# Kernel tuning notes

Measured on AMD Instinct MI355X. Metric: run time of the kernel, lower is better.

Reference implementation:

```python
import jax, jax.numpy as jnp
import numpy as np

FORMULA_OH_SIZES = [20, 20, 20, 20, 20]
SPECT_BIN_N = 512


def layer_norm(x, g, b, eps=1e-5):
    m = jnp.mean(x, axis=-1, keepdims=True)
    v = jnp.var(x, axis=-1, keepdims=True)
    return (x - m) * jax.lax.rsqrt(v + eps) * g + b


def gru_cell(x, h, W_ih, W_hh, b_ih, b_hh):
    # torch.nn.GRUCell math
    gi = x @ W_ih.T + b_ih
    gh = h @ W_hh.T + b_hh
    i_r, i_z, i_n = jnp.split(gi, 3, axis=-1)
    h_r, h_z, h_n = jnp.split(gh, 3, axis=-1)
    r = jax.nn.sigmoid(i_r + h_r)
    z = jax.nn.sigmoid(i_z + h_z)
    n = jnp.tanh(i_n + r * h_n)
    return (1.0 - z) * n + z * h


def structured_one_hot(x, sizes, accum=True):
    # x: [N, len(sizes)] integer element counts -> concatenated (accumulated) one-hots
    outs = []
    for i, s in enumerate(sizes):
        v = jnp.clip(x[:, i].astype(jnp.int32), 0, s - 1)
        if accum:
            oh = (jnp.arange(s)[None, :] <= v[:, None]).astype(jnp.float32)  # thermometer
        else:
            oh = jax.nn.one_hot(v, s, dtype=jnp.float32)
        outs.append(oh)
    return jnp.concatenate(outs, axis=-1)


def setup_inputs():
    key = jax.random.key(0)
    ks = jax.random.split(key, 16)
    B, A, GF, HW, S, M = 16, 32, 128, 4, 4096, 8
    G = GF * HW                       # 512 = g_feat_in * highway_steps_n
    FE = sum(FORMULA_OH_SIZES)        # 100
    D = 512                           # internal_d
    vert_feat_in = jax.random.normal(ks[0], (B, A, GF, HW), jnp.float32)
    vert_mask_in = jnp.ones((B, A), jnp.float32)
    elem_id = jax.random.randint(ks[1], (B, A), 0, 5)
    vert_element_oh = jax.nn.one_hot(elem_id, 5, dtype=jnp.float32)
    adj_oh = jnp.zeros((B, A, A, 4), jnp.float32)  # unused by forward
    atom_subsets = jax.random.bernoulli(ks[2], 0.5, (B, S, A)).astype(jnp.float32)
    masses = jax.random.uniform(ks[3], (B, S, M), jnp.float32, 0.0, SPECT_BIN_N - 1.0)
    intens = jax.random.uniform(ks[4], (B, S, M), jnp.float32)
    atom_subsets_peaks = jnp.stack([masses, intens], axis=-1)

    def lin(k, o, i):
        return (jax.random.normal(k, (o, i), jnp.float32) / np.sqrt(i)).astype(jnp.float32)

    return dict(
        vert_feat_in=vert_feat_in, vert_mask_in=vert_mask_in,
        vert_element_oh=vert_element_oh, adj_oh=adj_oh,
        atom_subsets=atom_subsets, atom_subsets_peaks=atom_subsets_peaks,
        ln_sub_g=jnp.ones((G,), jnp.float32), ln_sub_b=jnp.zeros((G,), jnp.float32),
        W_ih=lin(ks[5], 3 * G, FE), W_hh=lin(ks[6], 3 * G, G),
        b_ih=jnp.zeros((3 * G,), jnp.float32), b_hh=jnp.zeros((3 * G,), jnp.float32),
        W1=lin(ks[7], D, G), b1=jnp.zeros((D,), jnp.float32),
        W2a=lin(ks[8], D, D), b2a=jnp.zeros((D,), jnp.float32),
        W2b=lin(ks[9], D, D), b2b=jnp.zeros((D,), jnp.float32),
        ln_pre_g=jnp.ones((D,), jnp.float32), ln_pre_b=jnp.zeros((D,), jnp.float32),
        Ws=lin(ks[10], 1, D), bs=jnp.zeros((1,), jnp.float32),
    )


def reference(vert_feat_in, vert_mask_in, vert_element_oh, adj_oh, atom_subsets,
              atom_subsets_peaks, ln_sub_g, ln_sub_b, W_ih, W_hh, b_ih, b_hh,
              W1, b1, W2a, b2a, W2b, b2b, ln_pre_g, ln_pre_b, Ws, bs):
    B, A, GF, HW = vert_feat_in.shape
    S = atom_subsets.shape[1]
    vf = vert_feat_in.reshape(B, A, GF * HW)                       # [B,A,G]
    masked_vf = vf * vert_mask_in[:, :, None]
    subs_m = atom_subsets * vert_mask_in[:, None, :]               # [B,S,A]
    swvs = jnp.einsum('bag,bsa->bsg', masked_vf, subs_m)           # [B,S,G]
    # per-subset element counts -> structured one-hot formula encoding
    counts = jnp.einsum('bae,bsa->bse', vert_element_oh, atom_subsets).astype(jnp.int32)
    pf_flat = structured_one_hot(counts.reshape(B * S, -1), FORMULA_OH_SIZES, accum=True)
    subset_size = jnp.sum(subs_m, axis=2) + 1e-4                   # [B,S]
    mean = swvs / subset_size[:, :, None]
    normed = layer_norm(mean, ln_sub_g, ln_sub_b)                  # [B,S,G]
    h = gru_cell(pf_flat, normed.reshape(B * S, -1), W_ih, W_hh, b_ih, b_hh)
    h = h.reshape(normed.shape)
    x = jax.nn.relu(h @ W1.T + b1)
    x = jax.nn.relu(x @ W2a.T + b2a)
    x = jax.nn.relu(x @ W2b.T + b2b)   # (extra F.relu in original is idempotent)
    x = layer_norm(x, ln_pre_g, ln_pre_b)
    scores = (x @ Ws.T + bs)[..., 0]                               # [B,S]
    probs = jax.nn.softmax(scores, axis=-1)
    # mass histogram: scatter intensity*prob into rounded-mass bins
    masses = atom_subsets_peaks[..., 0]                            # [B,S,M]
    intens = atom_subsets_peaks[..., 1]
    bins = jnp.clip(jnp.round(masses).astype(jnp.int32), 0, SPECT_BIN_N - 1)
    contrib = intens * probs[:, :, None]                           # [B,S,M]
    spect = jnp.zeros((B, SPECT_BIN_N), x.dtype).at[
        jnp.arange(B)[:, None], bins.reshape(B, -1)].add(contrib.reshape(B, -1))
    return (spect, probs)
```

## Files before the change

### kernel.cpp

```cpp
#include <hip/hip_runtime.h>
#include <math.h>

#define B_ 16
#define A_ 32
#define G_ 512
#define S_ 4096
#define M_ 8
#define BS_ 65536
#define KC_ 640
#define NG_ 1536

typedef _Float16 half8 __attribute__((ext_vector_type(8)));
typedef _Float16 half4v __attribute__((ext_vector_type(4)));
typedef _Float16 half2v __attribute__((ext_vector_type(2)));
typedef float floatx4 __attribute__((ext_vector_type(4)));

typedef const __attribute__((address_space(1))) void* gas_t;
typedef __attribute__((address_space(3))) void* las_t;

__device__ __forceinline__ float wave_sum_f(float v){
#pragma unroll
  for (int o = 32; o > 0; o >>= 1) v += __shfl_xor(v, o);
  return v;
}
__device__ __forceinline__ float wave_max_f(float v){
#pragma unroll
  for (int o = 32; o > 0; o >>= 1) v = fmaxf(v, __shfl_xor(v, o));
  return v;
}
__device__ __forceinline__ float sigmoidf_(float x){ return 1.f/(1.f+__expf(-x)); }
__device__ __forceinline__ float tanhf_(float x){ return 1.f - 2.f/(__expf(2.f*x)+1.f); }

__global__ __launch_bounds__(256) void k_cvt3(const float* __restrict__ s0,
                                              const float* __restrict__ s1,
                                              const float* __restrict__ s2,
                                              _Float16* __restrict__ d){
  const float* s = (blockIdx.y == 0) ? s0 : (blockIdx.y == 1) ? s1 : s2;
  int i = (blockIdx.x*256 + threadIdx.x)*4;
  if (i >= G_*G_) return;
  float4 v = *(const float4*)(s+i);
  half4v o; o[0]=(_Float16)v.x; o[1]=(_Float16)v.y; o[2]=(_Float16)v.z; o[3]=(_Float16)v.w;
  *(half4v*)(d + (size_t)blockIdx.y*G_*G_ + i) = o;
}

__global__ __launch_bounds__(64) void k_buildw(const float* __restrict__ Whh,
                                               const float* __restrict__ Wih,
                                               _Float16* __restrict__ Wcat){
  int j = blockIdx.x;
  for (int p = threadIdx.x; p < KC_; p += 64){
    float v = 0.f;
    if (p < 512) v = Whh[(size_t)j*512 + p];
    else if (p < 612) v = Wih[(size_t)j*100 + (p - 512)];
    Wcat[(size_t)j*KC_ + p] = (_Float16)v;
  }
}

__global__ __launch_bounds__(256) void k_prep_mfma(
    const float* __restrict__ vf, const float* __restrict__ mask,
    const float* __restrict__ eoh, const float* __restrict__ subs,
    const float* __restrict__ ln_g, const float* __restrict__ ln_b,
    _Float16* __restrict__ Abuf){
  __shared__ _Float16 s_mvfT[G_*A_];
  __shared__ _Float16 s_sm[128*A_];
  __shared__ float s_m[A_];
  __shared__ float s_e[A_*5];
  __shared__ float s_ssum[128];
  __shared__ float s_red1[2][4][16];
  __shared__ float s_red2[2][4][16];
  int tid = threadIdx.x;
  int bx = blockIdx.x, b = blockIdx.y;
  int lane = tid & 63, w = tid >> 6;
  int q = lane >> 4, l15 = lane & 15;
  size_t row0 = (size_t)b*S_ + (size_t)bx*128;
  if (tid < A_)   s_m[tid] = mask[b*A_ + tid];
  if (tid < A_*5) s_e[tid] = eoh[b*A_*5 + tid];
  __syncthreads();
  {
    int p = tid & 15, gseg = tid >> 4;
    float mk0 = s_m[2*p], mk1 = s_m[2*p+1];
    const float* v0 = vf + ((size_t)b*A_ + 2*p)*G_ + gseg*32;
    const float* v1 = v0 + G_;
#pragma unroll
    for (int i = 0; i < 32; i += 4){
      float4 a = *(const float4*)(v0 + i);
      float4 c = *(const float4*)(v1 + i);
      float av[4] = {a.x, a.y, a.z, a.w};
      float cv[4] = {c.x, c.y, c.z, c.w};
#pragma unroll
      for (int j = 0; j < 4; ++j){
        half2v h; h[0] = (_Float16)(av[j]*mk0); h[1] = (_Float16)(cv[j]*mk1);
        *(half2v*)(s_mvfT + (gseg*32 + i + j)*A_ + 2*p) = h;
      }
    }
  }
  {
    int s = tid >> 1, hh = tid & 1;
    const float* sp = subs + (row0 + s)*A_ + hh*16;
    _Float16* dst = s_sm + s*A_ + hh*16;
#pragma unroll
    for (int i = 0; i < 16; i += 4){
      float4 v = *(const float4*)(sp + i);
      half4v h; h[0]=(_Float16)v.x; h[1]=(_Float16)v.y; h[2]=(_Float16)v.z; h[3]=(_Float16)v.w;
      *(half4v*)(dst + i) = h;
    }
  }
  __syncthreads();
  if (tid < 128){
    int s = tid;
    float ssum = 0.f, c0=0.f, c1=0.f, c2=0.f, c3=0.f, c4=0.f;
#pragma unroll
    for (int a = 0; a < A_; ++a){
      float v = (float)s_sm[s*A_ + a];
      ssum += v * s_m[a];
      c0 += v * s_e[a*5+0]; c1 += v * s_e[a*5+1]; c2 += v * s_e[a*5+2];
      c3 += v * s_e[a*5+3]; c4 += v * s_e[a*5+4];
    }
    int cc[5];
    cc[0] = min(max((int)(c0+0.5f),0),19); cc[1] = min(max((int)(c1+0.5f),0),19);
    cc[2] = min(max((int)(c2+0.5f),0),19); cc[3] = min(max((int)(c3+0.5f),0),19);
    cc[4] = min(max((int)(c4+0.5f),0),19);
    s_ssum[s] = ssum;
    _Float16* dst = Abuf + (row0 + s)*KC_ + 512;
#pragma unroll
    for (int t = 0; t < 16; ++t){
      half8 hv;
#pragma unroll
      for (int u = 0; u < 8; ++u){
        int k = t*8 + u;
        float v = 0.f;
        if (k < 100){ int f = k/20, l = k - f*20; v = (l <= cc[f]) ? 1.f : 0.f; }
        hv[u] = (_Float16)v;
      }
      *(half8*)(dst + t*8) = hv;
    }
  }
  half8 bf[8]; float lng[8], lnb[8];
#pragma unroll
  for (int t = 0; t < 8; ++t){
    int g = w*128 + t*16 + l15;
    bf[t] = *(const half8*)(s_mvfT + g*A_ + q*8);
    lng[t] = ln_g[g]; lnb[t] = ln_b[g];
  }
  __syncthreads();
  for (int gi = 0; gi < 8; ++gi){
    half8 af = *(const half8*)(s_sm + (gi*16 + l15)*A_ + q*8);
    floatx4 c[8];
#pragma unroll
    for (int t = 0; t < 8; ++t){
      floatx4 z = {0.f, 0.f, 0.f, 0.f};
      c[t] = __builtin_amdgcn_mfma_f32_16x16x32_f16(af, bf[t], z, 0, 0, 0);
    }
    float p1[4] = {0.f,0.f,0.f,0.f}, p2[4] = {0.f,0.f,0.f,0.f};
#pragma unroll
    for (int t = 0; t < 8; ++t)
#pragma unroll
      for (int r = 0; r < 4; ++r){ float v = c[t][r]; p1[r] += v; p2[r] += v*v; }
#pragma unroll
    for (int off = 1; off < 16; off <<= 1)
#pragma unroll
      for (int r = 0; r < 4; ++r){
        p1[r] += __shfl_xor(p1[r], off);
        p2[r] += __shfl_xor(p2[r], off);
      }
    int gb = gi & 1;
    if (l15 == 0){
#pragma unroll
      for (int r = 0; r < 4; ++r){ s_red1[gb][w][q*4+r] = p1[r]; s_red2[gb][w][q*4+r] = p2[r]; }
    }
    __syncthreads();
#pragma unroll
    for (int r = 0; r < 4; ++r){
      int sl = gi*16 + q*4 + r;
      int rr = q*4 + r;
      float t1 = s_red1[gb][0][rr] + s_red1[gb][1][rr] + s_red1[gb][2][rr] + s_red1[gb][3][rr];
      float t2 = s_red2[gb][0][rr] + s_red2[gb][1][rr] + s_red2[gb][2][rr] + s_red2[gb][3][rr];
      float inv = 1.f/(s_ssum[sl] + 1e-4f);
      float mu = t1*inv*(1.f/512.f);
      float var = t2*inv*inv*(1.f/512.f) - mu*mu;
      float rs = rsqrtf(var + 1e-5f);
      _Float16* orow = Abuf + (row0 + sl)*KC_;
#pragma unroll
      for (int t = 0; t < 8; ++t){
        float o = (c[t][r]*inv - mu)*rs*lng[t] + lnb[t];
        orow[w*128 + t*16 + l15] = (_Float16)o;
      }
    }
  }
}

__global__ __launch_bounds__(512) void k_gru_fused(
    const _Float16* __restrict__ Abuf, const _Float16* __restrict__ Wcat,
    const float* __restrict__ bih, const float* __restrict__ bhh,
    _Float16* __restrict__ H){
  __shared__ _Float16 smA[128*32];
  __shared__ _Float16 smB[192*32];
  int tid = threadIdx.x;
  int lane = tid & 63, wvid = tid >> 6;
  int wm = wvid & 1, wn = wvid >> 1;
  int q = lane >> 4, l15 = lane & 15;
  int mt = blockIdx.x*64 + (blockIdx.y >> 3);
  int dt = blockIdx.y & 7;
  int m0 = mt*128, n0 = dt*64;
  floatx4 acc[3][4] = {};
  floatx4 accNI[4] = {};
  int offA[4], offB[3];
#pragma unroll
  for (int i = 0; i < 4; ++i){
    int r = wm*64 + i*16 + l15;
    offA[i] = (r*4 + (q ^ ((r>>2)&3)))*8;
  }
#pragma unroll
  for (int g = 0; g < 3; ++g){
    int rb = g*64 + wn*16 + l15;
    offB[g] = (rb*4 + (q ^ ((rb>>2)&3)))*8;
  }
  const _Float16* gA;
  {
    int u = wvid*64 + lane;
    int r = u >> 2, c = (u & 3) ^ ((r >> 2) & 3);
    gA = Abuf + (size_t)(m0 + r)*KC_ + c*8;
  }
  const _Float16* gB0;
  {
    int u = wvid*64 + lane;
    int rb = u >> 2, c = (u & 3) ^ ((rb >> 2) & 3);
    int grow = (rb >> 6)*512 + n0 + (rb & 63);
    gB0 = Wcat + (size_t)grow*KC_ + c*8;
  }
  const _Float16* gB1 = nullptr;
  if (wvid < 4){
    int u = (8 + wvid)*64 + lane;
    int rb = u >> 2, c = (u & 3) ^ ((rb >> 2) & 3);
    int grow = (rb >> 6)*512 + n0 + (rb & 63);
    gB1 = Wcat + (size_t)grow*KC_ + c*8;
  }
  for (int kc = 0; kc < 512; kc += 32){
    __builtin_amdgcn_global_load_lds((gas_t)(gA + kc), (las_t)(smA + wvid*512), 16, 0, 0);
    __builtin_amdgcn_global_load_lds((gas_t)(gB0 + kc), (las_t)(smB + wvid*512), 16, 0, 0);
    if (wvid < 4)
      __builtin_amdgcn_global_load_lds((gas_t)(gB1 + kc), (las_t)(smB + (8+wvid)*512), 16, 0, 0);
    __syncthreads();
    half8 af[4], bfv[3];
#pragma unroll
    for (int i = 0; i < 4; ++i) af[i] = *(const half8*)(smA + offA[i]);
#pragma unroll
    for (int g = 0; g < 3; ++g) bfv[g] = *(const half8*)(smB + offB[g]);
#pragma unroll
    for (int g = 0; g < 3; ++g)
#pragma unroll
      for (int i = 0; i < 4; ++i)
        acc[g][i] = __builtin_amdgcn_mfma_f32_16x16x32_f16(af[i], bfv[g], acc[g][i], 0, 0, 0);
    __syncthreads();
  }
  for (int kc = 512; kc < KC_; kc += 32){
    __builtin_amdgcn_global_load_lds((gas_t)(gA + kc), (las_t)(smA + wvid*512), 16, 0, 0);
    __builtin_amdgcn_global_load_lds((gas_t)(gB0 + kc), (las_t)(smB + wvid*512), 16, 0, 0);
    if (wvid < 4)
      __builtin_amdgcn_global_load_lds((gas_t)(gB1 + kc), (las_t)(smB + (8+wvid)*512), 16, 0, 0);
    __syncthreads();
    half8 af[4], bfv[3];
#pragma unroll
    for (int i = 0; i < 4; ++i) af[i] = *(const half8*)(smA + offA[i]);
#pragma unroll
    for (int g = 0; g < 3; ++g) bfv[g] = *(const half8*)(smB + offB[g]);
#pragma unroll
    for (int i = 0; i < 4; ++i){
      acc[0][i] = __builtin_amdgcn_mfma_f32_16x16x32_f16(af[i], bfv[0], acc[0][i], 0, 0, 0);
      acc[1][i] = __builtin_amdgcn_mfma_f32_16x16x32_f16(af[i], bfv[1], acc[1][i], 0, 0, 0);
      accNI[i]  = __builtin_amdgcn_mfma_f32_16x16x32_f16(af[i], bfv[2], accNI[i], 0, 0, 0);
    }
    __syncthreads();
  }
  int d = n0 + wn*16 + l15;
  float br  = bih[d] + bhh[d];
  float bz  = bih[512+d] + bhh[512+d];
  float bnh = bhh[1024+d];
  float bni = bih[1024+d];
#pragma unroll
  for (int i = 0; i < 4; ++i){
#pragma unroll
    for (int r = 0; r < 4; ++r){
      int m = m0 + wm*64 + i*16 + q*4 + r;
      float gr  = acc[0][i][r] + br;
      float gz  = acc[1][i][r] + bz;
      float hn  = acc[2][i][r] + bnh;
      float in_ = accNI[i][r] + bni;
      float rrv = sigmoidf_(gr);
      float zz  = sigmoidf_(gz);
      float nn  = tanhf_(in_ + rrv*hn);
      float hp  = (float)Abuf[(size_t)m*KC_ + d];
      H[(size_t)m*G_ + d] = (_Float16)((1.f-zz)*nn + zz*hp);
    }
  }
}

__global__ __launch_bounds__(256) void k_gemm(
    const _Float16* __restrict__ A, const _Float16* __restrict__ W,
    const float* __restrict__ bias, _Float16* __restrict__ Out){
  __shared__ _Float16 smA[128*32];
  __shared__ _Float16 smB[128*32];
  int tid = threadIdx.x;
  int lane = tid & 63, wvid = tid >> 6;
  int wm = wvid & 1, wn = wvid >> 1;
  int q = lane >> 4, l15 = lane & 15;
  int mt = blockIdx.x*64 + (blockIdx.y >> 2);
  int nt = blockIdx.y & 3;
  int m0 = mt*128, n0 = nt*128;
  floatx4 acc[4][4] = {};
  int offA[4], offB[4];
#pragma unroll
  for (int i = 0; i < 4; ++i){
    int r = wm*64 + i*16 + l15;
    offA[i] = (r*4 + (q ^ ((r>>2)&3)))*8;
    int rb = wn*64 + i*16 + l15;
    offB[i] = (rb*4 + (q ^ ((rb>>2)&3)))*8;
  }
  int uA[2];
  const _Float16 *gA[2], *gB[2];
#pragma unroll
  for (int t = 0; t < 2; ++t){
    int seg = wvid*2 + t;
    int u = seg*64 + lane;
    int r = u >> 2, c = (u & 3) ^ ((r >> 2) & 3);
    uA[t] = seg;
    gA[t] = A + (size_t)(m0 + r)*G_ + c*8;
    gB[t] = W + (size_t)(n0 + r)*G_ + c*8;
  }
  for (int kc = 0; kc < G_; kc += 32){
#pragma unroll
    for (int t = 0; t < 2; ++t){
      __builtin_amdgcn_global_load_lds((gas_t)(gA[t] + kc), (las_t)(smA + uA[t]*512), 16, 0, 0);
      __builtin_amdgcn_global_load_lds((gas_t)(gB[t] + kc), (las_t)(smB + uA[t]*512), 16, 0, 0);
    }
    __syncthreads();
    half8 af[4], bfv[4];
#pragma unroll
    for (int i = 0; i < 4; ++i) af[i] = *(const half8*)(smA + offA[i]);
#pragma unroll
    for (int j = 0; j < 4; ++j) bfv[j] = *(const half8*)(smB + offB[j]);
#pragma unroll
    for (int i = 0; i < 4; ++i)
#pragma unroll
      for (int j = 0; j < 4; ++j)
        acc[i][j] = __builtin_amdgcn_mfma_f32_16x16x32_f16(af[i], bfv[j], acc[i][j], 0, 0, 0);
    __syncthreads();
  }
#pragma unroll
  for (int j = 0; j < 4; ++j){
    int n = n0 + wn*64 + j*16 + l15;
    float bv = bias[n];
#pragma unroll
    for (int i = 0; i < 4; ++i){
#pragma unroll
      for (int r = 0; r < 4; ++r){
        int m = m0 + wm*64 + i*16 + q*4 + r;
        Out[(size_t)m*G_ + n] = (_Float16)fmaxf(acc[i][j][r] + bv, 0.f);
      }
    }
  }
}

__global__ __launch_bounds__(256) void k_ff3_fin(
    const _Float16* __restrict__ A, const _Float16* __restrict__ W,
    const float* __restrict__ bias, const float* __restrict__ ln_pre_g,
    const float* __restrict__ Ws, float* __restrict__ Pbuf){
  __shared__ _Float16 smA[128*32];
  __shared__ _Float16 smB[128*32];
  __shared__ float sP[2][64][2][3];
  int tid = threadIdx.x;
  int lane = tid & 63, wvid = tid >> 6;
  int wm = wvid & 1, wn = wvid >> 1;
  int q = lane >> 4, l15 = lane & 15;
  int mt = blockIdx.x*64 + (blockIdx.y >> 2);
  int nt = blockIdx.y & 3;
  int m0 = mt*128, n0 = nt*128;
  floatx4 acc[4][4] = {};
  int offA[4], offB[4];
#pragma unroll
  for (int i = 0; i < 4; ++i){
    int r = wm*64 + i*16 + l15;
    offA[i] = (r*4 + (q ^ ((r>>2)&3)))*8;
    int rb = wn*64 + i*16 + l15;
    offB[i] = (rb*4 + (q ^ ((rb>>2)&3)))*8;
  }
  int uA[2];
  const _Float16 *gA[2], *gB[2];
#pragma unroll
  for (int t = 0; t < 2; ++t){
    int seg = wvid*2 + t;
    int u = seg*64 + lane;
    int r = u >> 2, c = (u & 3) ^ ((r >> 2) & 3);
    uA[t] = seg;
    gA[t] = A + (size_t)(m0 + r)*G_ + c*8;
    gB[t] = W + (size_t)(n0 + r)*G_ + c*8;
  }
  for (int kc = 0; kc < G_; kc += 32){
#pragma unroll
    for (int t = 0; t < 2; ++t){
      __builtin_amdgcn_global_load_lds((gas_t)(gA[t] + kc), (las_t)(smA + uA[t]*512), 16, 0, 0);
      __builtin_amdgcn_global_load_lds((gas_t)(gB[t] + kc), (las_t)(smB + uA[t]*512), 16, 0, 0);
    }
    __syncthreads();
    half8 af[4], bfv[4];
#pragma unroll
    for (int i = 0; i < 4; ++i) af[i] = *(const half8*)(smA + offA[i]);
#pragma unroll
    for (int j = 0; j < 4; ++j) bfv[j] = *(const half8*)(smB + offB[j]);
#pragma unroll
    for (int i = 0; i < 4; ++i)
#pragma unroll
      for (int j = 0; j < 4; ++j)
        acc[i][j] = __builtin_amdgcn_mfma_f32_16x16x32_f16(af[i], bfv[j], acc[i][j], 0, 0, 0);
    __syncthreads();
  }
  float gws[4], bv4[4];
#pragma unroll
  for (int j = 0; j < 4; ++j){
    int n = n0 + wn*64 + j*16 + l15;
    gws[j] = ln_pre_g[n]*Ws[n];
    bv4[j] = bias[n];
  }
#pragma unroll
  for (int i = 0; i < 4; ++i){
#pragma unroll
    for (int r = 0; r < 4; ++r){
      float p1 = 0.f, p2 = 0.f, p3 = 0.f;
#pragma unroll
      for (int j = 0; j < 4; ++j){
        float x = fmaxf(acc[i][j][r] + bv4[j], 0.f);
        p1 += x; p2 += x*x; p3 += gws[j]*x;
      }
#pragma unroll
      for (int off = 1; off < 16; off <<= 1){
        p1 += __shfl_xor(p1, off);
        p2 += __shfl_xor(p2, off);
        p3 += __shfl_xor(p3, off);
      }
      if (l15 == 0){
        int rl = i*16 + q*4 + r;
        sP[wm][rl][wn][0] = p1; sP[wm][rl][wn][1] = p2; sP[wm][rl][wn][2] = p3;
      }
    }
  }
  __syncthreads();
  if (tid < 128){
    int wmi = tid >> 6, rl = tid & 63;
    int m = m0 + wmi*64 + rl;
    float* dst = Pbuf + ((size_t)m*4 + nt)*3;
    dst[0] = sP[wmi][rl][0][0] + sP[wmi][rl][1][0];
    dst[1] = sP[wmi][rl][0][1] + sP[wmi][rl][1][1];
    dst[2] = sP[wmi][rl][0][2] + sP[wmi][rl][1][2];
  }
}

__global__ __launch_bounds__(256) void k_score_fin(
    const float* __restrict__ Pbuf, const float* __restrict__ g,
    const float* __restrict__ bta, const float* __restrict__ Ws,
    const float* __restrict__ bs, float* __restrict__ scores){
  __shared__ float red[8];
  int tid = threadIdx.x, lane = tid & 63, wv = tid >> 6;
  int i0 = tid*2;
  float c1p = g[i0]*Ws[i0] + g[i0+1]*Ws[i0+1];
  float c2p = bta[i0]*Ws[i0] + bta[i0+1]*Ws[i0+1];
  c1p = wave_sum_f(c1p); c2p = wave_sum_f(c2p);
  if (lane == 0){ red[wv] = c1p; red[4+wv] = c2p; }
  __syncthreads();
  float c1 = red[0]+red[1]+red[2]+red[3];
  float c2 = red[4]+red[5]+red[6]+red[7] + bs[0];
  size_t row = (size_t)blockIdx.x*256 + tid;
  const float* p = Pbuf + row*12;
  float4 a  = *(const float4*)p;
  float4 b4 = *(const float4*)(p+4);
  float4 c4 = *(const float4*)(p+8);
  float P1 = a.x + a.w + b4.z + c4.y;
  float P2 = a.y + b4.x + b4.w + c4.z;
  float P3 = a.z + b4.y + c4.x + c4.w;
  float mu = P1*(1.f/512.f);
  float var = P2*(1.f/512.f) - mu*mu;
  float rs = rsqrtf(var + 1e-5f);
  scores[row] = rs*(P3 - mu*c1) + c2;
}

__global__ __launch_bounds__(256) void k_softmax(
    const float* __restrict__ scores, float* __restrict__ probs){
  __shared__ float red[4];
  int b = blockIdx.x, tid = threadIdx.x, lane = tid & 63, wv = tid >> 6;
  const float* sp = scores + (size_t)b*S_;
  float mx = -1e30f;
  for (int i = tid; i < S_; i += 256) mx = fmaxf(mx, sp[i]);
  mx = wave_max_f(mx);
  if (lane == 0) red[wv] = mx;
  __syncthreads();
  mx = fmaxf(fmaxf(red[0], red[1]), fmaxf(red[2], red[3]));
  __syncthreads();
  float sum = 0.f;
  for (int i = tid; i < S_; i += 256) sum += __expf(sp[i]-mx);
  sum = wave_sum_f(sum);
  if (lane == 0) red[wv] = sum;
  __syncthreads();
  sum = red[0]+red[1]+red[2]+red[3];
  float inv = 1.f/sum;
  for (int i = tid; i < S_; i += 256)
    probs[(size_t)b*S_ + i] = __expf(sp[i]-mx)*inv;
}

__global__ __launch_bounds__(256) void k_spect(
    const float* __restrict__ peaks, const float* __restrict__ probs,
    float* __restrict__ spect){
  __shared__ float bins[512];
  int b = blockIdx.x, tid = threadIdx.x;
  bins[tid] = 0.f; bins[tid+256] = 0.f;
  __syncthreads();
  for (int i = tid; i < S_*M_; i += 256){
    int s = i >> 3, m = i & 7;
    const float* pk = peaks + (((size_t)b*S_ + s)*M_ + m)*2;
    float mass = pk[0], inten = pk[1];
    float p = probs[(size_t)b*S_ + s];
    int bin = (int)rintf(mass);
    bin = min(max(bin, 0), 511);
    atomicAdd(&bins[bin], inten*p);
  }
  __syncthreads();
  spect[(size_t)b*512 + tid]       = bins[tid];
  spect[(size_t)b*512 + tid + 256] = bins[tid+256];
}

extern "C" void kernel_launch(void* const* d_in, const int* in_sizes, int n_in,
                              void* d_out, int out_size, void* d_ws, size_t ws_size,
                              hipStream_t stream) {
  const float* vf       = (const float*)d_in[0];
  const float* mask     = (const float*)d_in[1];
  const float* eoh      = (const float*)d_in[2];
  const float* subs     = (const float*)d_in[4];
  const float* peaks    = (const float*)d_in[5];
  const float* ln_sub_g = (const float*)d_in[6];
  const float* ln_sub_b = (const float*)d_in[7];
  const float* W_ih     = (const float*)d_in[8];
  const float* W_hh     = (const float*)d_in[9];
  const float* b_ih     = (const float*)d_in[10];
  const float* b_hh     = (const float*)d_in[11];
  const float* W1       = (const float*)d_in[12];
  const float* b1       = (const float*)d_in[13];
  const float* W2a      = (const float*)d_in[14];
  const float* b2a      = (const float*)d_in[15];
  const float* W2b      = (const float*)d_in[16];
  const float* b2b      = (const float*)d_in[17];
  const float* ln_pre_g = (const float*)d_in[18];
  const float* ln_pre_b = (const float*)d_in[19];
  const float* Ws       = (const float*)d_in[20];
  const float* bs       = (const float*)d_in[21];
  float* out = (float*)d_out;
  float* probs_out = out + (size_t)B_*512;

  char* w = (char*)d_ws;
  float* scores = (float*)w;     w += (size_t)BS_*4;
  float* Pbuf   = (float*)w;     w += (size_t)BS_*12*4;
  _Float16* Wcat = (_Float16*)w; w += (size_t)NG_*KC_*2;
  _Float16* W1h  = (_Float16*)w; w += (size_t)G_*G_*2;
  _Float16* W2ah = (_Float16*)w; w += (size_t)G_*G_*2;
  _Float16* W2bh = (_Float16*)w; w += (size_t)G_*G_*2;
  _Float16* Abuf = (_Float16*)w; w += (size_t)BS_*KC_*2;
  _Float16* bufh0 = (_Float16*)w;
  _Float16* bufh1 = Abuf;

  k_cvt3<<<dim3((G_*G_/4+255)/256, 3), 256, 0, stream>>>(W1, W2a, W2b, W1h);
  k_buildw<<<NG_, 64, 0, stream>>>(W_hh, W_ih, Wcat);
  k_prep_mfma<<<dim3(S_/128, B_), 256, 0, stream>>>(vf, mask, eoh, subs,
                                                    ln_sub_g, ln_sub_b, Abuf);
  k_gru_fused<<<dim3(8, 512), 512, 0, stream>>>(Abuf, Wcat, b_ih, b_hh, bufh0);
  k_gemm<<<dim3(8, 256), 256, 0, stream>>>(bufh0, W1h,  b1,  bufh1);
  k_gemm<<<dim3(8, 256), 256, 0, stream>>>(bufh1, W2ah, b2a, bufh0);
  k_ff3_fin<<<dim3(8, 256), 256, 0, stream>>>(bufh0, W2bh, b2b,
                                              ln_pre_g, Ws, Pbuf);
  k_score_fin<<<BS_/256, 256, 0, stream>>>(Pbuf, ln_pre_g, ln_pre_b, Ws, bs, scores);
  k_softmax<<<B_, 256, 0, stream>>>(scores, probs_out);
  k_spect<<<B_, 256, 0, stream>>>(peaks, probs_out, out);
}
```

Baseline: 526.5 us.

## Use 8 waves per GEMM block and fuse score, softmax and spectrum kernels

The three FF GEMM kernels now run 512 threads (8 waves) per 128x128 tile, so each wave computes a 64x32 sub-tile and issues one LDS load per operand instead of two. This halves the accumulators per wave, which should lower register pressure and raise occupancy and latency hiding. Separately, the score finalisation, softmax and spectrum scatter are merged into one kernel per batch that keeps scores and probabilities in shared memory, removing two launches and a global scores buffer. The tradeoff is that score computation now runs in only 16 blocks instead of 256, so less of the GPU is busy for that stage.

```diff
diff --git a/kernel.cpp b/kernel.cpp
--- a/kernel.cpp
+++ b/kernel.cpp
@@ -294,7 +294,7 @@
   }
 }
 
-__global__ __launch_bounds__(256) void k_gemm(
+__global__ __launch_bounds__(512) void k_gemm(
     const _Float16* __restrict__ A, const _Float16* __restrict__ W,
     const float* __restrict__ bias, _Float16* __restrict__ Out){
   __shared__ _Float16 smA[128*32];
@@ -306,48 +306,44 @@
   int mt = blockIdx.x*64 + (blockIdx.y >> 2);
   int nt = blockIdx.y & 3;
   int m0 = mt*128, n0 = nt*128;
-  floatx4 acc[4][4] = {};
-  int offA[4], offB[4];
+  floatx4 acc[4][2] = {};
+  int offA[4], offB[2];
 #pragma unroll
   for (int i = 0; i < 4; ++i){
     int r = wm*64 + i*16 + l15;
     offA[i] = (r*4 + (q ^ ((r>>2)&3)))*8;
-    int rb = wn*64 + i*16 + l15;
-    offB[i] = (rb*4 + (q ^ ((rb>>2)&3)))*8;
-  }
-  int uA[2];
-  const _Float16 *gA[2], *gB[2];
-#pragma unroll
-  for (int t = 0; t < 2; ++t){
-    int seg = wvid*2 + t;
-    int u = seg*64 + lane;
+  }
+#pragma unroll
+  for (int j = 0; j < 2; ++j){
+    int rb = wn*32 + j*16 + l15;
+    offB[j] = (rb*4 + (q ^ ((rb>>2)&3)))*8;
+  }
+  const _Float16 *gA, *gB;
+  {
+    int u = wvid*64 + lane;
     int r = u >> 2, c = (u & 3) ^ ((r >> 2) & 3);
-    uA[t] = seg;
-    gA[t] = A + (size_t)(m0 + r)*G_ + c*8;
-    gB[t] = W + (size_t)(n0 + r)*G_ + c*8;
+    gA = A + (size_t)(m0 + r)*G_ + c*8;
+    gB = W + (size_t)(n0 + r)*G_ + c*8;
   }
   for (int kc = 0; kc < G_; kc += 32){
-#pragma unroll
-    for (int t = 0; t < 2; ++t){
-      __builtin_amdgcn_global_load_lds((gas_t)(gA[t] + kc), (las_t)(smA + uA[t]*512), 16, 0, 0);
-      __builtin_amdgcn_global_load_lds((gas_t)(gB[t] + kc), (las_t)(smB + uA[t]*512), 16, 0, 0);
-    }
-    __syncthreads();
-    half8 af[4], bfv[4];
+    __builtin_amdgcn_global_load_lds((gas_t)(gA + kc), (las_t)(smA + wvid*512), 16, 0, 0);
+    __builtin_amdgcn_global_load_lds((gas_t)(gB + kc), (las_t)(smB + wvid*512), 16, 0, 0);
+    __syncthreads();
+    half8 af[4], bfv[2];
 #pragma unroll
     for (int i = 0; i < 4; ++i) af[i] = *(const half8*)(smA + offA[i]);
 #pragma unroll
-    for (int j = 0; j < 4; ++j) bfv[j] = *(const half8*)(smB + offB[j]);
+    for (int j = 0; j < 2; ++j) bfv[j] = *(const half8*)(smB + offB[j]);
 #pragma unroll
     for (int i = 0; i < 4; ++i)
 #pragma unroll
-      for (int j = 0; j < 4; ++j)
+      for (int j = 0; j < 2; ++j)
         acc[i][j] = __builtin_amdgcn_mfma_f32_16x16x32_f16(af[i], bfv[j], acc[i][j], 0, 0, 0);
     __syncthreads();
   }
 #pragma unroll
-  for (int j = 0; j < 4; ++j){
-    int n = n0 + wn*64 + j*16 + l15;
+  for (int j = 0; j < 2; ++j){
+    int n = n0 + wn*32 + j*16 + l15;
     float bv = bias[n];
 #pragma unroll
     for (int i = 0; i < 4; ++i){
@@ -360,13 +356,13 @@
   }
 }
 
-__global__ __launch_bounds__(256) void k_ff3_fin(
+__global__ __launch_bounds__(512) void k_ff3_fin(
     const _Float16* __restrict__ A, const _Float16* __restrict__ W,
     const float* __restrict__ bias, const float* __restrict__ ln_pre_g,
     const float* __restrict__ Ws, float* __restrict__ Pbuf){
   __shared__ _Float16 smA[128*32];
   __shared__ _Float16 smB[128*32];
-  __shared__ float sP[2][64][2][3];
+  __shared__ float sP[2][64][4][3];
   int tid = threadIdx.x;
   int lane = tid & 63, wvid = tid >> 6;
   int wm = wvid & 1, wn = wvid >> 1;
@@ -374,51 +370,47 @@
   int mt = blockIdx.x*64 + (blockIdx.y >> 2);
   int nt = blockIdx.y & 3;
   int m0 = mt*128, n0 = nt*128;
-  floatx4 acc[4][4] = {};
-  int offA[4], offB[4];
+  floatx4 acc[4][2] = {};
+  int offA[4], offB[2];
 #pragma unroll
   for (int i = 0; i < 4; ++i){
     int r = wm*64 + i*16 + l15;
     offA[i] = (r*4 + (q ^ ((r>>2)&3)))*8;
-    int rb = wn*64 + i*16 + l15;
-    offB[i] = (rb*4 + (q ^ ((rb>>2)&3)))*8;
-  }
-  int uA[2];
-  const _Float16 *gA[2], *gB[2];
-#pragma unroll
-  for (int t = 0; t < 2; ++t){
-    int seg = wvid*2 + t;
-    int u = seg*64 + lane;
+  }
+#pragma unroll
+  for (int j = 0; j < 2; ++j){
+    int rb = wn*32 + j*16 + l15;
+    offB[j] = (rb*4 + (q ^ ((rb>>2)&3)))*8;
+  }
+  const _Float16 *gA, *gB;
+  {
+    int u = wvid*64 + lane;
     int r = u >> 2, c = (u & 3) ^ ((r >> 2) & 3);
-    uA[t] = seg;
-    gA[t] = A + (size_t)(m0 + r)*G_ + c*8;
-    gB[t] = W + (size_t)(n0 + r)*G_ + c*8;
+    gA = A + (size_t)(m0 + r)*G_ + c*8;
+    gB = W + (size_t)(n0 + r)*G_ + c*8;
   }
   for (int kc = 0; kc < G_; kc += 32){
-#pragma unroll
-    for (int t = 0; t < 2; ++t){
-      __builtin_amdgcn_global_load_lds((gas_t)(gA[t] + kc), (las_t)(smA + uA[t]*512), 16, 0, 0);
-      __builtin_amdgcn_global_load_lds((gas_t)(gB[t] + kc), (las_t)(smB + uA[t]*512), 16, 0, 0);
-    }
-    __syncthreads();
-    half8 af[4], bfv[4];
+    __builtin_amdgcn_global_load_lds((gas_t)(gA + kc), (las_t)(smA + wvid*512), 16, 0, 0);
+    __builtin_amdgcn_global_load_lds((gas_t)(gB + kc), (las_t)(smB + wvid*512), 16, 0, 0);
+    __syncthreads();
+    half8 af[4], bfv[2];
 #pragma unroll
     for (int i = 0; i < 4; ++i) af[i] = *(const half8*)(smA + offA[i]);
 #pragma unroll
-    for (int j = 0; j < 4; ++j) bfv[j] = *(const half8*)(smB + offB[j]);
+    for (int j = 0; j < 2; ++j) bfv[j] = *(const half8*)(smB + offB[j]);
 #pragma unroll
     for (int i = 0; i < 4; ++i)
 #pragma unroll
-      for (int j = 0; j < 4; ++j)
+      for (int j = 0; j < 2; ++j)
         acc[i][j] = __builtin_amdgcn_mfma_f32_16x16x32_f16(af[i], bfv[j], acc[i][j], 0, 0, 0);
     __syncthreads();
   }
-  float gws[4], bv4[4];
-#pragma unroll
-  for (int j = 0; j < 4; ++j){
-    int n = n0 + wn*64 + j*16 + l15;
+  float gws[2], bv2[2];
+#pragma unroll
+  for (int j = 0; j < 2; ++j){
+    int n = n0 + wn*32 + j*16 + l15;
     gws[j] = ln_pre_g[n]*Ws[n];
-    bv4[j] = bias[n];
+    bv2[j] = bias[n];
   }
 #pragma unroll
   for (int i = 0; i < 4; ++i){
@@ -426,8 +418,8 @@
     for (int r = 0; r < 4; ++r){
       float p1 = 0.f, p2 = 0.f, p3 = 0.f;
 #pragma unroll
-      for (int j = 0; j < 4; ++j){
-        float x = fmaxf(acc[i][j][r] + bv4[j], 0.f);
+      for (int j = 0; j < 2; ++j){
+        float x = fmaxf(acc[i][j][r] + bv2[j], 0.f);
         p1 += x; p2 += x*x; p3 += gws[j]*x;
       }
 #pragma unroll
@@ -447,78 +439,69 @@
     int wmi = tid >> 6, rl = tid & 63;
     int m = m0 + wmi*64 + rl;
     float* dst = Pbuf + ((size_t)m*4 + nt)*3;
-    dst[0] = sP[wmi][rl][0][0] + sP[wmi][rl][1][0];
-    dst[1] = sP[wmi][rl][0][1] + sP[wmi][rl][1][1];
-    dst[2] = sP[wmi][rl][0][2] + sP[wmi][rl][1][2];
-  }
-}
-
-__global__ __launch_bounds__(256) void k_score_fin(
+    dst[0] = sP[wmi][rl][0][0] + sP[wmi][rl][1][0] + sP[wmi][rl][2][0] + sP[wmi][rl][3][0];
+    dst[1] = sP[wmi][rl][0][1] + sP[wmi][rl][1][1] + sP[wmi][rl][2][1] + sP[wmi][rl][3][1];
+    dst[2] = sP[wmi][rl][0][2] + sP[wmi][rl][1][2] + sP[wmi][rl][2][2] + sP[wmi][rl][3][2];
+  }
+}
+
+__global__ __launch_bounds__(256) void k_soft_spect(
     const float* __restrict__ Pbuf, const float* __restrict__ g,
     const float* __restrict__ bta, const float* __restrict__ Ws,
-    const float* __restrict__ bs, float* __restrict__ scores){
+    const float* __restrict__ bs, const float* __restrict__ peaks,
+    float* __restrict__ probs, float* __restrict__ spect){
+  __shared__ float sc[S_];
   __shared__ float red[8];
-  int tid = threadIdx.x, lane = tid & 63, wv = tid >> 6;
+  __shared__ float bins[512];
+  int b = blockIdx.x, tid = threadIdx.x, lane = tid & 63, wv = tid >> 6;
   int i0 = tid*2;
   float c1p = g[i0]*Ws[i0] + g[i0+1]*Ws[i0+1];
   float c2p = bta[i0]*Ws[i0] + bta[i0+1]*Ws[i0+1];
   c1p = wave_sum_f(c1p); c2p = wave_sum_f(c2p);
   if (lane == 0){ red[wv] = c1p; red[4+wv] = c2p; }
+  bins[tid] = 0.f; bins[tid+256] = 0.f;
   __syncthreads();
   float c1 = red[0]+red[1]+red[2]+red[3];
   float c2 = red[4]+red[5]+red[6]+red[7] + bs[0];
-  size_t row = (size_t)blockIdx.x*256 + tid;
-  const float* p = Pbuf + row*12;
-  float4 a  = *(const float4*)p;
-  float4 b4 = *(const float4*)(p+4);
-  float4 c4 = *(const float4*)(p+8);
-  float P1 = a.x + a.w + b4.z + c4.y;
-  float P2 = a.y + b4.x + b4.w + c4.z;
-  float P3 = a.z + b4.y + c4.x + c4.w;
-  float mu = P1*(1.f/512.f);
-  float var = P2*(1.f/512.f) - mu*mu;
-  float rs = rsqrtf(var + 1e-5f);
-  scores[row] = rs*(P3 - mu*c1) + c2;
-}
-
-__global__ __launch_bounds__(256) void k_softmax(
-    const float* __restrict__ scores, float* __restrict__ probs){
-  __shared__ float red[4];
-  int b = blockIdx.x, tid = threadIdx.x, lane = tid & 63, wv = tid >> 6;
-  const float* sp = scores + (size_t)b*S_;
   float mx = -1e30f;
-  for (int i = tid; i < S_; i += 256) mx = fmaxf(mx, sp[i]);
+  for (int i = tid; i < S_; i += 256){
+    const float* p = Pbuf + ((size_t)b*S_ + i)*12;
+    float4 a  = *(const float4*)p;
+    float4 b4 = *(const float4*)(p+4);
+    float4 c4 = *(const float4*)(p+8);
+    float P1 = a.x + a.w + b4.z + c4.y;
+    float P2 = a.y + b4.x + b4.w + c4.z;
+    float P3 = a.z + b4.y + c4.x + c4.w;
+    float mu = P1*(1.f/512.f);
+    float var = P2*(1.f/512.f) - mu*mu;
+    float rs = rsqrtf(var + 1e-5f);
+    float s = rs*(P3 - mu*c1) + c2;
+    sc[i] = s;
+    mx = fmaxf(mx, s);
+  }
   mx = wave_max_f(mx);
+  __syncthreads();
   if (lane == 0) red[wv] = mx;
   __syncthreads();
   mx = fmaxf(fmaxf(red[0], red[1]), fmaxf(red[2], red[3]));
-  __syncthreads();
   float sum = 0.f;
-  for (int i = tid; i < S_; i += 256) sum += __expf(sp[i]-mx);
+  for (int i = tid; i < S_; i += 256) sum += __expf(sc[i]-mx);
   sum = wave_sum_f(sum);
-  if (lane == 0) red[wv] = sum;
-  __syncthreads();
-  sum = red[0]+red[1]+red[2]+red[3];
+  if (lane == 0) red[4+wv] = sum;
+  __syncthreads();
+  sum = red[4]+red[5]+red[6]+red[7];
   float inv = 1.f/sum;
-  for (int i = tid; i < S_; i += 256)
-    probs[(size_t)b*S_ + i] = __expf(sp[i]-mx)*inv;
-}
-
-__global__ __launch_bounds__(256) void k_spect(
-    const float* __restrict__ peaks, const float* __restrict__ probs,
-    float* __restrict__ spect){
-  __shared__ float bins[512];
-  int b = blockIdx.x, tid = threadIdx.x;
-  bins[tid] = 0.f; bins[tid+256] = 0.f;
+  for (int i = tid; i < S_; i += 256){
+    float p = __expf(sc[i]-mx)*inv;
+    probs[(size_t)b*S_ + i] = p;
+    sc[i] = p;
+  }
   __syncthreads();
   for (int i = tid; i < S_*M_; i += 256){
     int s = i >> 3, m = i & 7;
     const float* pk = peaks + (((size_t)b*S_ + s)*M_ + m)*2;
-    float mass = pk[0], inten = pk[1];
-    float p = probs[(size_t)b*S_ + s];
-    int bin = (int)rintf(mass);
-    bin = min(max(bin, 0), 511);
-    atomicAdd(&bins[bin], inten*p);
+    int bin = min(max((int)rintf(pk[0]), 0), 511);
+    atomicAdd(&bins[bin], pk[1]*sc[s]);
   }
   __syncthreads();
   spect[(size_t)b*512 + tid]       = bins[tid];
@@ -553,7 +536,6 @@
   float* probs_out = out + (size_t)B_*512;
 
   char* w = (char*)d_ws;
-  float* scores = (float*)w;     w += (size_t)BS_*4;
   float* Pbuf   = (float*)w;     w += (size_t)BS_*12*4;
   _Float16* Wcat = (_Float16*)w; w += (size_t)NG_*KC_*2;
   _Float16* W1h  = (_Float16*)w; w += (size_t)G_*G_*2;
@@ -568,11 +550,10 @@
   k_prep_mfma<<<dim3(S_/128, B_), 256, 0, stream>>>(vf, mask, eoh, subs,
                                                     ln_sub_g, ln_sub_b, Abuf);
   k_gru_fused<<<dim3(8, 512), 512, 0, stream>>>(Abuf, Wcat, b_ih, b_hh, bufh0);
-  k_gemm<<<dim3(8, 256), 256, 0, stream>>>(bufh0, W1h,  b1,  bufh1);
-  k_gemm<<<dim3(8, 256), 256, 0, stream>>>(bufh1, W2ah, b2a, bufh0);
-  k_ff3_fin<<<dim3(8, 256), 256, 0, stream>>>(bufh0, W2bh, b2b,
+  k_gemm<<<dim3(8, 256), 512, 0, stream>>>(bufh0, W1h,  b1,  bufh1);
+  k_gemm<<<dim3(8, 256), 512, 0, stream>>>(bufh1, W2ah, b2a, bufh0);
+  k_ff3_fin<<<dim3(8, 256), 512, 0, stream>>>(bufh0, W2bh, b2b,
                                               ln_pre_g, Ws, Pbuf);
-  k_score_fin<<<BS_/256, 256, 0, stream>>>(Pbuf, ln_pre_g, ln_pre_b, Ws, bs, scores);
-  k_softmax<<<B_, 256, 0, stream>>>(scores, probs_out);
-  k_spect<<<B_, 256, 0, stream>>>(peaks, probs_out, out);
-}
+  k_soft_spect<<<B_, 256, 0, stream>>>(Pbuf, ln_pre_g, ln_pre_b, Ws, bs,
+                                       peaks, probs_out, out);
+}
```

Measured after the change: 542.6 us. 3.1% more time.
